# Optimization experiments

Hardware: AMD Instinct MI355X
Metric: run time of the kernel (lower is better)

Reference implementation:

```python
import jax, jax.numpy as jnp
import numpy as np

V, EMB, HID, ENC = 32000, 512, 1024, 1024
B, T, TB = 64, 512, 512
PAD = 0


def setup_inputs() -> dict:
    key = jax.random.key(0)
    kk = jax.random.split(key, 24)
    w = lambda k, s: jax.random.normal(k, s, dtype=jnp.float32) * 0.02
    a = lambda k, s: jax.random.normal(k, s, dtype=jnp.float32)
    emb_table = w(kk[0], (V, EMB)).at[PAD].set(0.0)  # padding_idx row zeroed
    IN = EMB + ENC + HID  # lstm input size
    return {
        "y": jax.random.randint(kk[1], (B,), 0, V),
        "h": a(kk[2], (B, HID)),
        "c": a(kk[3], (B, HID)),
        "enc_out": a(kk[4], (B, T, ENC)),
        "bwd_states": a(kk[5], (B, TB, HID)),
        "src_ids": jax.random.randint(kk[6], (B, T), 0, V),
        "src_mask": jnp.ones((B, T), dtype=jnp.int32),
        "emb_table": emb_table,
        "W_ih": w(kk[7], (4 * HID, IN)),
        "W_hh": w(kk[8], (4 * HID, HID)),
        "b_ih": jnp.zeros((4 * HID,), jnp.float32),
        "b_hh": jnp.zeros((4 * HID,), jnp.float32),
        "Wq_e": w(kk[9], (HID, HID)),
        "Wk_e": w(kk[10], (HID, ENC)),
        "v_e": w(kk[11], (HID,)),
        "Wq_b": w(kk[12], (HID, HID)),
        "Wk_b": w(kk[13], (HID, HID)),
        "v_b": w(kk[14], (HID,)),
        "Wp": w(kk[15], (V, HID)),
        "bp": jnp.zeros((V,), jnp.float32),
        "wc": w(kk[16], (ENC,)),
        "ws": w(kk[17], (HID,)),
        "wy": w(kk[18], (EMB,)),
        "pg_b": jnp.zeros((), jnp.float32),
    }


def _bahdanau(query, keys, Wq, Wk, v, mask=None):
    # query [B,H], keys [B,T,D] -> context [B,D], attn [B,T]
    q = query @ Wq.T                                  # [B,A]
    k = jnp.einsum("btd,ad->bta", keys, Wk)           # [B,T,A]
    e = jnp.einsum("bta,a->bt", jnp.tanh(q[:, None, :] + k), v)
    if mask is not None:
        e = jnp.where(mask == 0, jnp.finfo(e.dtype).min, e)
    attn = jax.nn.softmax(e, axis=-1)
    ctx = jnp.einsum("bt,btd->bd", attn, keys)
    return ctx, attn


def reference(y, h, c, enc_out, bwd_states, src_ids, src_mask, emb_table,
              W_ih, W_hh, b_ih, b_hh, Wq_e, Wk_e, v_e, Wq_b, Wk_b, v_b,
              Wp, bp, wc, ws, wy, pg_b):
    emb = emb_table[y]                                # [B,EMB]
    query = h                                         # state[0].squeeze(0)
    c_enc, attn_enc = _bahdanau(query, enc_out, Wq_e, Wk_e, v_e, src_mask)
    c_bwd, _ = _bahdanau(query, bwd_states, Wq_b, Wk_b, v_b)
    x = jnp.concatenate([emb, c_enc, c_bwd], axis=-1)  # [B,EMB+ENC+HID]
    gates = x @ W_ih.T + h @ W_hh.T + b_ih + b_hh      # [B,4H], torch order i,f,g,o
    i, f, g, o = jnp.split(gates, 4, axis=-1)
    c_new = jax.nn.sigmoid(f) * c + jax.nn.sigmoid(i) * jnp.tanh(g)
    h_new = jax.nn.sigmoid(o) * jnp.tanh(c_new)
    vocab_dist = jax.nn.softmax(h_new @ Wp.T + bp, axis=-1)  # [B,V]
    p_gen = jax.nn.sigmoid(c_enc @ wc + h_new @ ws + emb @ wy + pg_b)[:, None]
    p_vocab = p_gen * vocab_dist
    copy_mask = (src_ids < V).astype(vocab_dist.dtype)
    safe_ids = jnp.minimum(src_ids, V - 1)
    contrib = (1.0 - p_gen) * attn_enc * copy_mask     # [B,T]
    scatter = jax.vmap(lambda idx, val: jnp.zeros((V,), val.dtype).at[idx].add(val))(safe_ids, contrib)
    final_dist = p_vocab + scatter
    return final_dist, h_new, c_new
```

## Files before the change

### kernel.cpp

```cpp
#include <hip/hip_runtime.h>
#include <hip/hip_bf16.h>

#define VSZ   32000
#define EMBD  512
#define HIDD  1024
#define BB    64
#define TSEQ  512
#define G4    4096

typedef short bf16x8 __attribute__((ext_vector_type(8)));
typedef float f32x4  __attribute__((ext_vector_type(4)));

typedef __attribute__((address_space(3))) unsigned       lds_u32_t;
typedef __attribute__((address_space(1))) const unsigned glb_u32_t;
__device__ __forceinline__ void gload16(const void* g, void* l){
  __builtin_amdgcn_global_load_lds((glb_u32_t*)g, (lds_u32_t*)l, 16, 0, 0);
}

__device__ __forceinline__ float sigmoid_f(float x){ return 1.0f/(1.0f+__expf(-x)); }
__device__ __forceinline__ float fast_tanh(float x){
  float e = __expf(2.0f*x);
  return 1.0f - 2.0f*__builtin_amdgcn_rcpf(e + 1.0f);
}
__device__ __forceinline__ short f2bfs(float x){
  unsigned u = __float_as_uint(x);
  unsigned r = (u + 0x7FFFu + ((u>>16)&1u)) >> 16;
  return (short)r;
}
__device__ __forceinline__ float bf2f(short s){
  return __uint_as_float(((unsigned)(unsigned short)s) << 16);
}
__device__ __forceinline__ unsigned cvtpk(float a, float b){
  unsigned r;
  asm("v_cvt_pk_bf16_f32 %0, %1, %2" : "=v"(r) : "v"(a), "v"(b));
  return r;
}
__device__ __forceinline__ bf16x8 cvt8(float4 a, float4 b){
  union { unsigned u[4]; bf16x8 v; } o;
  o.u[0]=cvtpk(a.x,a.y); o.u[1]=cvtpk(a.z,a.w);
  o.u[2]=cvtpk(b.x,b.y); o.u[3]=cvtpk(b.z,b.w);
  return o.v;
}
__device__ __forceinline__ float wave_sum(float x){
  #pragma unroll
  for (int off=32; off>0; off>>=1) x += __shfl_xor(x, off);
  return x;
}
__device__ __forceinline__ float wave_max(float x){
  #pragma unroll
  for (int off=32; off>0; off>>=1) x = fmaxf(x, __shfl_xor(x, off));
  return x;
}

__global__ __launch_bounds__(256) void k_pack(const float* __restrict__ Wk,
                                              short* __restrict__ dst){
  int id = blockIdx.x*256 + threadIdx.x;
  int a = id >> 7, g = id & 127;
  int gs = (g & ~7) | ((g & 7) ^ (a & 7));
  const float* src = Wk + (size_t)a*1024 + gs*8;
  float4 f0 = ((const float4*)src)[0], f1 = ((const float4*)src)[1];
  *(bf16x8*)(dst + (size_t)id*8) = cvt8(f0, f1);
}

__global__ __launch_bounds__(256) void k_cvtkeys(const float* __restrict__ enc,
                                                 const float* __restrict__ bwd,
                                                 short* __restrict__ dst){
  int att = blockIdx.y;
  const float* src0 = att ? bwd : enc;
  int id = blockIdx.x*256 + threadIdx.x;
  int g = id & 127, bt = id >> 7;
  int t = bt & 511;
  int gs = (g & ~7) | ((g & 7) ^ (t & 7));
  const float* sp = src0 + (size_t)bt*1024 + gs*8;
  float4 f0 = ((const float4*)sp)[0], f1 = ((const float4*)sp)[1];
  *(bf16x8*)(dst + (((size_t)att*32768 + bt)*128 + g)*8) = cvt8(f0, f1);
}

__global__ __launch_bounds__(256) void k_prep_h(const float* __restrict__ h,
                                                short* __restrict__ xb){
  int id = blockIdx.x*256 + threadIdx.x;
  int b = id >> 7, d = (id & 127)*8;
  const float4* s = (const float4*)(h + (size_t)b*HIDD + d);
  *(bf16x8*)(xb + (size_t)b*3584 + 2560 + d) = cvt8(s[0], s[1]);
}

__global__ __launch_bounds__(256) void k_prep_x2(const float* __restrict__ tab,
                                                 const int* __restrict__ y,
                                                 const float* __restrict__ ctxe,
                                                 const float* __restrict__ ctxb,
                                                 short* __restrict__ xb){
  int id = blockIdx.x*256 + threadIdx.x;
  if (id >= 64*320) return;
  int b = id / 320, off = (id % 320)*8;
  const float* src;
  if (off < 512)        src = tab  + (size_t)y[b]*EMBD + off;
  else if (off < 1536)  src = ctxe + (size_t)b*HIDD + (off-512);
  else                  src = ctxb + (size_t)b*HIDD + (off-1536);
  float4 f0 = ((const float4*)src)[0], f1 = ((const float4*)src)[1];
  *(bf16x8*)(xb + (size_t)b*3584 + off) = cvt8(f0, f1);
}

__global__ __launch_bounds__(256) void k_mm64(
    const short* __restrict__ A0, int lda0, const float* __restrict__ B0, int ldb0, int K0, float* __restrict__ out0, int ldo0,
    const short* __restrict__ A1, int lda1, const float* __restrict__ B1, int ldb1, int K1, float* __restrict__ out1, int ldo1){
  const short* A; const float* B; float* out; int lda, ldb, K, ldo;
  if (blockIdx.z == 0){ A=A0; B=B0; out=out0; lda=lda0; ldb=ldb0; K=K0; ldo=ldo0; }
  else                { A=A1; B=B1; out=out1; lda=lda1; ldb=ldb1; K=K1; ldo=ldo1; }
  int tid = threadIdx.x, l = tid & 63, w = tid >> 6;
  int l15 = l & 15, l4 = l >> 4;
  int n0 = blockIdx.x*256 + w*64;
  int kper = K / gridDim.y;
  int dbeg = blockIdx.y * kper, dend = dbeg + kper;
  f32x4 acc[4][4];
  #pragma unroll
  for (int i=0;i<4;i++)
    #pragma unroll
    for (int j=0;j<4;j++)
      #pragma unroll
      for (int r=0;r<4;r++) acc[i][j][r]=0.f;
  for (int d0=dbeg; d0<dend; d0+=32){
    bf16x8 af[4];
    #pragma unroll
    for (int ms=0; ms<4; ms++)
      af[ms] = *(const bf16x8*)(A + (size_t)(ms*16 + l15)*lda + d0 + l4*8);
    bf16x8 bfr[4];
    #pragma unroll
    for (int ni=0; ni<4; ni++){
      const float* bp = B + (size_t)(n0 + ni*16 + l15)*ldb + d0 + l4*8;
      float4 f0 = ((const float4*)bp)[0], f1 = ((const float4*)bp)[1];
      bfr[ni] = cvt8(f0, f1);
    }
    #pragma unroll
    for (int ms=0; ms<4; ms++)
      #pragma unroll
      for (int ni=0; ni<4; ni++)
        acc[ms][ni] = __builtin_amdgcn_mfma_f32_16x16x32_bf16(af[ms], bfr[ni], acc[ms][ni], 0,0,0);
  }
  float* op = out + (size_t)blockIdx.y * 64 * ldo;
  #pragma unroll
  for (int ms=0; ms<4; ms++)
    #pragma unroll
    for (int ni=0; ni<4; ni++)
      #pragma unroll
      for (int r=0; r<4; r++){
        int m = ms*16 + l4*4 + r;
        op[(size_t)m*ldo + n0 + ni*16 + l15] = acc[ms][ni][r];
      }
}

__global__ __launch_bounds__(256,3) void k_energy(
    const short* __restrict__ pkeys,
    const short* __restrict__ pke, const short* __restrict__ pkb,
    const float* __restrict__ qpe, const float* __restrict__ qpb,
    const float* __restrict__ ve, const float* __restrict__ vb,
    float* __restrict__ ep_out){
  __shared__ short A_s[128*64];
  __shared__ short B_s[128*64];
  __shared__ float ebuf[2][128];

  int wg = blockIdx.x;
  int xcd = wg & 7, idx = wg >> 3;
  int tglob = xcd*64 + (idx >> 3);
  int A0 = idx & 7;
  int att = tglob >> 8;
  int tt  = tglob & 255;
  int b = tt >> 2, t0 = (tt & 3)*128;

  const short* pk = att ? pkb : pke;
  const float* qp = att ? qpb : qpe;
  const float* v  = att ? vb  : ve;

  int tid = threadIdx.x, l = tid & 63, w = tid >> 6;
  int l15 = l & 15, l4 = l >> 4;
  int wr = w >> 1, wc = w & 1;

  const char* asrc = (const char*)(pkeys + ((size_t)att*32768 + (size_t)b*512)*1024)
                   + (size_t)(t0 + w*32 + (l>>3))*2048 + (l&7)*16;
  const char* bsrc = (const char*)pk + (size_t)(A0*128 + w*32 + (l>>3))*2048 + (l&7)*16;

  f32x4 acc[4][4];
  #pragma unroll
  for (int i=0;i<4;i++)
    #pragma unroll
    for (int j=0;j<4;j++)
      #pragma unroll
      for (int r=0;r<4;r++) acc[i][j][r]=0.f;

  for (int c=0; c<16; ++c){
    if (c) __syncthreads();
    #pragma unroll
    for (int k=0;k<4;k++)
      gload16(asrc + (size_t)c*128 + (size_t)k*16384, (char*)A_s + w*4096 + k*1024);
    #pragma unroll
    for (int k=0;k<4;k++)
      gload16(bsrc + (size_t)c*128 + (size_t)k*16384, (char*)B_s + w*4096 + k*1024);
    __syncthreads();
    #pragma unroll
    for (int ks=0; ks<2; ks++){
      bf16x8 af[4], bf[4];
      #pragma unroll
      for (int ms=0; ms<4; ms++){
        int row = wr*64 + ms*16 + l15;
        af[ms] = *(const bf16x8*)((char*)A_s + row*128 + ((ks*64 + l4*16) ^ ((row&7)<<4)));
      }
      #pragma unroll
      for (int ni=0; ni<4; ni++){
        int row = wc*64 + ni*16 + l15;
        bf[ni] = *(const bf16x8*)((char*)B_s + row*128 + ((ks*64 + l4*16) ^ ((row&7)<<4)));
      }
      #pragma unroll
      for (int ms=0; ms<4; ms++)
        #pragma unroll
        for (int ni=0; ni<4; ni++)
          acc[ms][ni] = __builtin_amdgcn_mfma_f32_16x16x32_bf16(af[ms], bf[ni], acc[ms][ni], 0,0,0);
    }
  }

  float qv[4], vv[4];
  #pragma unroll
  for (int ni=0; ni<4; ni++){
    int a = A0*128 + wc*64 + ni*16 + l15;
    qv[ni] = qp[(size_t)b*HIDD + a] + qp[65536 + (size_t)b*HIDD + a];
    vv[ni] = v[a];
  }
  float es[16];
  #pragma unroll
  for (int ms=0; ms<4; ms++)
    #pragma unroll
    for (int r=0; r<4; r++){
      float s = 0.f;
      #pragma unroll
      for (int ni=0; ni<4; ni++)
        s += vv[ni]*fast_tanh(qv[ni] + acc[ms][ni][r]);
      es[ms*4+r] = s;
    }
  #pragma unroll
  for (int i=0;i<16;i++){
    float x = es[i];
    x += __shfl_xor(x,1); x += __shfl_xor(x,2);
    x += __shfl_xor(x,4); x += __shfl_xor(x,8);
    es[i] = x;
  }
  if (l15 == 0){
    #pragma unroll
    for (int ms=0; ms<4; ms++)
      #pragma unroll
      for (int r=0; r<4; r++)
        ebuf[wc][wr*64 + ms*16 + l4*4 + r] = es[ms*4+r];
  }
  __syncthreads();
  if (tid < 128)
    ep_out[(((size_t)att*8 + A0)*BB + b)*TSEQ + t0 + tid] = ebuf[0][tid] + ebuf[1][tid];
}

__global__ __launch_bounds__(256) void k_softmax_t(const float* __restrict__ ep,
                                                   const int* __restrict__ mask,
                                                   float* __restrict__ att_e,
                                                   float* __restrict__ att_b){
  int b = blockIdx.x, att = blockIdx.y;
  float* e = (att ? att_b : att_e) + (size_t)b*TSEQ;
  __shared__ float red[8];
  int tid = threadIdx.x, lane = tid & 63, w = tid >> 6;
  float v0 = 0.f, v1 = 0.f;
  #pragma unroll
  for (int i=0;i<8;i++){
    const float* p = ep + (((size_t)att*8 + i)*BB + b)*TSEQ;
    v0 += p[tid]; v1 += p[tid+256];
  }
  if (att==0){
    if (mask[(size_t)b*TSEQ + tid]==0)      v0 = -3.4e38f;
    if (mask[(size_t)b*TSEQ + tid+256]==0)  v1 = -3.4e38f;
  }
  float m = wave_max(fmaxf(v0, v1));
  if (lane==0) red[w] = m;
  __syncthreads();
  m = fmaxf(fmaxf(red[0],red[1]), fmaxf(red[2],red[3]));
  float x0 = __expf(v0-m), x1 = __expf(v1-m);
  float s = wave_sum(x0+x1);
  if (lane==0) red[4+w] = s;
  __syncthreads();
  s = red[4]+red[5]+red[6]+red[7];
  float inv = 1.0f/s;
  e[tid] = x0*inv; e[tid+256] = x1*inv;
}

__global__ __launch_bounds__(256) void k_ctx(const short* __restrict__ pkeys,
                                             const float* __restrict__ att_e,
                                             const float* __restrict__ att_b,
                                             float* __restrict__ ctxp){
  int b = blockIdx.x, sel = blockIdx.y, s = blockIdx.z;
  const short* base = pkeys + (((size_t)sel*32768) + (size_t)b*512 + s*64)*1024;
  const float* att  = (sel ? att_b : att_e) + (size_t)b*TSEQ + s*64;
  int g = threadIdx.x & 127, th = threadIdx.x >> 7;
  const short* rp = base + (size_t)th*32*1024;
  float acc[8];
  #pragma unroll
  for (int j=0;j<8;j++) acc[j]=0.f;
  for (int t=0;t<32;t++){
    float a = att[th*32 + t];
    int gg = (g & ~7) | ((g & 7) ^ (t & 7));
    bf16x8 kv = *(const bf16x8*)(rp + (size_t)t*1024 + gg*8);
    #pragma unroll
    for (int j=0;j<8;j++) acc[j] += a*bf2f(kv[j]);
  }
  float* o = ctxp + ((((size_t)sel*BB + b)*16) + s*2 + th)*1024 + g*8;
  float4 o0, o1;
  o0.x=acc[0]; o0.y=acc[1]; o0.z=acc[2]; o0.w=acc[3];
  o1.x=acc[4]; o1.y=acc[5]; o1.z=acc[6]; o1.w=acc[7];
  ((float4*)o)[0] = o0; ((float4*)o)[1] = o1;
}

__global__ __launch_bounds__(256) void k_ctxred(const float* __restrict__ ctxp,
                                                float* __restrict__ ctx_e,
                                                float* __restrict__ ctx_b){
  int id = blockIdx.x*256 + threadIdx.x;
  int sel = id >> 16; int rem = id & 65535; int b = rem >> 10; int d = rem & 1023;
  const float* p = ctxp + (((size_t)sel*BB + b)*16)*1024 + d;
  float s = 0.f;
  #pragma unroll
  for (int i=0;i<16;i++) s += p[i*1024];
  (sel ? ctx_b : ctx_e)[(size_t)b*HIDD + d] = s;
}

__global__ __launch_bounds__(256) void k_lstm(const float* __restrict__ gp,
                                              const float* __restrict__ b_ih,
                                              const float* __restrict__ b_hh,
                                              const float* __restrict__ c_old,
                                              float* __restrict__ out,
                                              short* __restrict__ hb){
  int id = blockIdx.x*256 + threadIdx.x;
  int b = id >> 10, j = id & 1023;
  size_t base = (size_t)b*G4;
  float gs[4];
  #pragma unroll
  for (int g=0; g<4; g++){
    int col = g*1024 + j;
    float s = b_ih[col] + b_hh[col];
    #pragma unroll
    for (int k=0;k<8;k++) s += gp[(size_t)k*(64*G4) + base + col];
    gs[g] = s;
  }
  float ig = sigmoid_f(gs[0]);
  float fg = sigmoid_f(gs[1]);
  float gg = tanhf(gs[2]);
  float og = sigmoid_f(gs[3]);
  float cn = fg*c_old[id] + ig*gg;
  float hn = og*tanhf(cn);
  out[(size_t)BB*VSZ + id] = hn;
  out[(size_t)BB*VSZ + (size_t)BB*HIDD + id] = cn;
  hb[id] = f2bfs(hn);
}

__global__ __launch_bounds__(256) void k_vocab2(const short* __restrict__ hb,
                                                const float* __restrict__ Wp,
                                                const float* __restrict__ bp,
                                                float* __restrict__ out){
  int tid = threadIdx.x, l = tid & 63, w = tid >> 6;
  int l15 = l & 15, l4 = l >> 4;
  int mh = w >> 1;
  int n0 = blockIdx.x*128 + (w&1)*64;
  f32x4 acc[2][4];
  #pragma unroll
  for (int i=0;i<2;i++)
    #pragma unroll
    for (int j=0;j<4;j++)
      #pragma unroll
      for (int r=0;r<4;r++) acc[i][j][r]=0.f;
  for (int d0=0; d0<1024; d0+=32){
    bf16x8 af[2];
    #pragma unroll
    for (int ms=0; ms<2; ms++)
      af[ms] = *(const bf16x8*)(hb + (size_t)(mh*32 + ms*16 + l15)*1024 + d0 + l4*8);
    bf16x8 bfr[4];
    #pragma unroll
    for (int ni=0; ni<4; ni++){
      const float* bpp = Wp + (size_t)(n0 + ni*16 + l15)*1024 + d0 + l4*8;
      float4 f0 = ((const float4*)bpp)[0], f1 = ((const float4*)bpp)[1];
      bfr[ni] = cvt8(f0, f1);
    }
    #pragma unroll
    for (int ms=0; ms<2; ms++)
      #pragma unroll
      for (int ni=0; ni<4; ni++)
        acc[ms][ni] = __builtin_amdgcn_mfma_f32_16x16x32_bf16(af[ms], bfr[ni], acc[ms][ni], 0,0,0);
  }
  #pragma unroll
  for (int ms=0; ms<2; ms++)
    #pragma unroll
    for (int ni=0; ni<4; ni++)
      #pragma unroll
      for (int r=0; r<4; r++){
        int m = mh*32 + ms*16 + l4*4 + r;
        int n = n0 + ni*16 + l15;
        out[(size_t)m*VSZ + n] = acc[ms][ni][r] + bp[n];
      }
}

__global__ __launch_bounds__(1024) void k_final(const float* __restrict__ ctxe,
                                                const float* __restrict__ tab,
                                                const int* __restrict__ y,
                                                const float* __restrict__ wc,
                                                const float* __restrict__ wsv,
                                                const float* __restrict__ wy,
                                                const float* __restrict__ pgb,
                                                float* __restrict__ out,
                                                float* __restrict__ pgen_ws){
  __shared__ float red[32];
  int b = blockIdx.x, tid = threadIdx.x, lane = tid & 63, w = tid >> 6;
  const float* hn = out + (size_t)BB*VSZ + (size_t)b*HIDD;
  float acc = ctxe[(size_t)b*HIDD + tid]*wc[tid] + hn[tid]*wsv[tid];
  if (tid < 512) acc += tab[(size_t)y[b]*EMBD + tid]*wy[tid];
  acc = wave_sum(acc);
  if (lane==0) red[w] = acc;
  __syncthreads();
  float s0 = pgb[0];
  #pragma unroll
  for (int i=0;i<16;i++) s0 += red[i];
  float pg = sigmoid_f(s0);
  if (tid==0) pgen_ws[b] = pg;
  __syncthreads();

  float* row = out + (size_t)b*VSZ;
  float m = -3.4e38f;
  for (int i=tid;i<VSZ;i+=1024) m = fmaxf(m, row[i]);
  m = wave_max(m);
  if (lane==0) red[w] = m;
  __syncthreads();
  #pragma unroll
  for (int i=0;i<16;i++) m = fmaxf(m, red[i]);
  float s = 0.f;
  for (int i=tid;i<VSZ;i+=1024) s += __expf(row[i]-m);
  s = wave_sum(s);
  if (lane==0) red[16+w] = s;
  __syncthreads();
  float tot = 0.f;
  #pragma unroll
  for (int i=0;i<16;i++) tot += red[16+i];
  float scale = pg / tot;
  for (int i=tid;i<VSZ;i+=1024) row[i] = __expf(row[i]-m)*scale;
}

__global__ __launch_bounds__(256) void k_scatter(const int* __restrict__ src_ids,
                                                 const float* __restrict__ att_e,
                                                 const float* __restrict__ pgen_ws,
                                                 float* __restrict__ out){
  int id = blockIdx.x*256 + threadIdx.x;
  int b = id >> 9;
  float pg = pgen_ws[b];
  int sid = src_ids[id];
  float contrib = (1.0f - pg) * att_e[id] * (sid < VSZ ? 1.0f : 0.0f);
  int safe = sid < VSZ-1 ? sid : VSZ-1;
  atomicAdd(&out[(size_t)b*VSZ + safe], contrib);
}

extern "C" void kernel_launch(void* const* d_in, const int* in_sizes, int n_in,
                              void* d_out, int out_size, void* d_ws, size_t ws_size,
                              hipStream_t stream){
  const int*   y     = (const int*)d_in[0];
  const float* h     = (const float*)d_in[1];
  const float* c     = (const float*)d_in[2];
  const float* enc   = (const float*)d_in[3];
  const float* bwd   = (const float*)d_in[4];
  const int*   sids  = (const int*)d_in[5];
  const int*   smask = (const int*)d_in[6];
  const float* tab   = (const float*)d_in[7];
  const float* W_ih  = (const float*)d_in[8];
  const float* W_hh  = (const float*)d_in[9];
  const float* b_ih  = (const float*)d_in[10];
  const float* b_hh  = (const float*)d_in[11];
  const float* Wq_e  = (const float*)d_in[12];
  const float* Wk_e  = (const float*)d_in[13];
  const float* v_e   = (const float*)d_in[14];
  const float* Wq_b  = (const float*)d_in[15];
  const float* Wk_b  = (const float*)d_in[16];
  const float* v_b   = (const float*)d_in[17];
  const float* Wp    = (const float*)d_in[18];
  const float* bp    = (const float*)d_in[19];
  const float* wc    = (const float*)d_in[20];
  const float* wsv   = (const float*)d_in[21];
  const float* wy    = (const float*)d_in[22];
  const float* pgb   = (const float*)d_in[23];
  float* out = (float*)d_out;

  float* W = (float*)d_ws;
  float* ws_qpe  = W; W += 2*BB*HIDD;
  float* ws_qpb  = W; W += 2*BB*HIDD;
  float* ws_ep   = W; W += 2*8*BB*TSEQ;
  float* ws_atte = W; W += BB*TSEQ;
  float* ws_attb = W; W += BB*TSEQ;
  float* ws_ctxe = W; W += BB*HIDD;
  float* ws_ctxb = W; W += BB*HIDD;
  float* ws_ctxp = W; W += 2*BB*16*1024;
  float* ws_pgen = W; W += 64;
  float* ws_gp   = W; W += 8*BB*G4;
  short* xb      = (short*)W; W += (BB*3584)/2;
  short* hb      = (short*)W; W += (BB*HIDD)/2;
  short* pk_e    = (short*)W; W += (HIDD*HIDD)/2;
  short* pk_b    = (short*)W; W += (HIDD*HIDD)/2;
  short* pkeys   = (short*)W; W += (2*BB*TSEQ*HIDD)/2;

  k_pack<<<512, 256, 0, stream>>>(Wk_e, pk_e);
  k_pack<<<512, 256, 0, stream>>>(Wk_b, pk_b);
  k_cvtkeys<<<dim3(16384,2), 256, 0, stream>>>(enc, bwd, pkeys);
  k_prep_h<<<32, 256, 0, stream>>>(h, xb);
  k_mm64<<<dim3(4,2,2), 256, 0, stream>>>(
      xb+2560, 3584, Wq_e, 1024, 1024, ws_qpe, 1024,
      xb+2560, 3584, Wq_b, 1024, 1024, ws_qpb, 1024);
  k_energy<<<4096, 256, 0, stream>>>(pkeys, pk_e, pk_b,
      ws_qpe, ws_qpb, v_e, v_b, ws_ep);
  k_softmax_t<<<dim3(BB,2), 256, 0, stream>>>(ws_ep, smask, ws_atte, ws_attb);
  k_ctx<<<dim3(BB,2,8), 256, 0, stream>>>(pkeys, ws_atte, ws_attb, ws_ctxp);
  k_ctxred<<<512, 256, 0, stream>>>(ws_ctxp, ws_ctxe, ws_ctxb);
  k_prep_x2<<<80, 256, 0, stream>>>(tab, y, ws_ctxe, ws_ctxb, xb);
  k_mm64<<<dim3(16,4,2), 256, 0, stream>>>(
      xb,      3584, W_ih, 2560, 2560, ws_gp,             G4,
      xb+2560, 3584, W_hh, 1024, 1024, ws_gp + 4*BB*G4,   G4);
  k_lstm<<<256, 256, 0, stream>>>(ws_gp, b_ih, b_hh, c, out, hb);
  k_vocab2<<<250, 256, 0, stream>>>(hb, Wp, bp, out);
  k_final<<<BB, 1024, 0, stream>>>(ws_ctxe, tab, y, wc, wsv, wy, pgb, out, ws_pgen);
  k_scatter<<<128, 256, 0, stream>>>(sids, ws_atte, ws_pgen, out);
}
```

Baseline: 391.6 us.

## Merge prep kernels and split vocab softmax into segmented reduce and scale

```diff
diff --git a/kernel.cpp b/kernel.cpp
--- a/kernel.cpp
+++ b/kernel.cpp
@@ -52,36 +52,39 @@
   return x;
 }
 
-__global__ __launch_bounds__(256) void k_pack(const float* __restrict__ Wk,
-                                              short* __restrict__ dst){
-  int id = blockIdx.x*256 + threadIdx.x;
-  int a = id >> 7, g = id & 127;
-  int gs = (g & ~7) | ((g & 7) ^ (a & 7));
-  const float* src = Wk + (size_t)a*1024 + gs*8;
-  float4 f0 = ((const float4*)src)[0], f1 = ((const float4*)src)[1];
-  *(bf16x8*)(dst + (size_t)id*8) = cvt8(f0, f1);
-}
-
-__global__ __launch_bounds__(256) void k_cvtkeys(const float* __restrict__ enc,
-                                                 const float* __restrict__ bwd,
-                                                 short* __restrict__ dst){
-  int att = blockIdx.y;
-  const float* src0 = att ? bwd : enc;
-  int id = blockIdx.x*256 + threadIdx.x;
-  int g = id & 127, bt = id >> 7;
-  int t = bt & 511;
-  int gs = (g & ~7) | ((g & 7) ^ (t & 7));
-  const float* sp = src0 + (size_t)bt*1024 + gs*8;
-  float4 f0 = ((const float4*)sp)[0], f1 = ((const float4*)sp)[1];
-  *(bf16x8*)(dst + (((size_t)att*32768 + bt)*128 + g)*8) = cvt8(f0, f1);
-}
-
-__global__ __launch_bounds__(256) void k_prep_h(const float* __restrict__ h,
-                                                short* __restrict__ xb){
-  int id = blockIdx.x*256 + threadIdx.x;
-  int b = id >> 7, d = (id & 127)*8;
-  const float4* s = (const float4*)(h + (size_t)b*HIDD + d);
-  *(bf16x8*)(xb + (size_t)b*3584 + 2560 + d) = cvt8(s[0], s[1]);
+__global__ __launch_bounds__(256) void k_prep_all(
+    const float* __restrict__ Wk_e, const float* __restrict__ Wk_b,
+    const float* __restrict__ enc,  const float* __restrict__ bwd,
+    const float* __restrict__ h,
+    short* __restrict__ pk_e, short* __restrict__ pk_b,
+    short* __restrict__ pkeys, short* __restrict__ xb){
+  int bid = blockIdx.x;
+  if (bid < 1024){
+    const float* Wk = (bid < 512) ? Wk_e : Wk_b;
+    short* dst      = (bid < 512) ? pk_e : pk_b;
+    int id = (bid & 511)*256 + threadIdx.x;
+    int a = id >> 7, g = id & 127;
+    int gs = (g & ~7) | ((g & 7) ^ (a & 7));
+    const float* src = Wk + (size_t)a*1024 + gs*8;
+    float4 f0 = ((const float4*)src)[0], f1 = ((const float4*)src)[1];
+    *(bf16x8*)(dst + (size_t)id*8) = cvt8(f0, f1);
+  } else if (bid < 33792){
+    int r = bid - 1024;
+    int att = r >> 14;
+    const float* src0 = att ? bwd : enc;
+    int id = (r & 16383)*256 + threadIdx.x;
+    int g = id & 127, bt = id >> 7;
+    int t = bt & 511;
+    int gs = (g & ~7) | ((g & 7) ^ (t & 7));
+    const float* sp = src0 + (size_t)bt*1024 + gs*8;
+    float4 f0 = ((const float4*)sp)[0], f1 = ((const float4*)sp)[1];
+    *(bf16x8*)(pkeys + (((size_t)att*32768 + bt)*128 + g)*8) = cvt8(f0, f1);
+  } else {
+    int id = (bid - 33792)*256 + threadIdx.x;
+    int b = id >> 7, d = (id & 127)*8;
+    const float4* s = (const float4*)(h + (size_t)b*HIDD + d);
+    *(bf16x8*)(xb + (size_t)b*3584 + 2560 + d) = cvt8(s[0], s[1]);
+  }
 }
 
 __global__ __launch_bounds__(256) void k_prep_x2(const float* __restrict__ tab,
@@ -396,48 +399,76 @@
       }
 }
 
-__global__ __launch_bounds__(1024) void k_final(const float* __restrict__ ctxe,
-                                                const float* __restrict__ tab,
-                                                const int* __restrict__ y,
-                                                const float* __restrict__ wc,
-                                                const float* __restrict__ wsv,
-                                                const float* __restrict__ wy,
-                                                const float* __restrict__ pgb,
-                                                float* __restrict__ out,
-                                                float* __restrict__ pgen_ws){
-  __shared__ float red[32];
+__global__ __launch_bounds__(256) void k_pgen(const float* __restrict__ ctxe,
+                                              const float* __restrict__ tab,
+                                              const int* __restrict__ y,
+                                              const float* __restrict__ wc,
+                                              const float* __restrict__ wsv,
+                                              const float* __restrict__ wy,
+                                              const float* __restrict__ pgb,
+                                              const float* __restrict__ out,
+                                              float* __restrict__ pgen_ws){
+  __shared__ float red[4];
   int b = blockIdx.x, tid = threadIdx.x, lane = tid & 63, w = tid >> 6;
   const float* hn = out + (size_t)BB*VSZ + (size_t)b*HIDD;
-  float acc = ctxe[(size_t)b*HIDD + tid]*wc[tid] + hn[tid]*wsv[tid];
-  if (tid < 512) acc += tab[(size_t)y[b]*EMBD + tid]*wy[tid];
+  const float* emb = tab + (size_t)y[b]*EMBD;
+  float acc = 0.f;
+  #pragma unroll
+  for (int i=0;i<4;i++){
+    int d = i*256 + tid;
+    acc += ctxe[(size_t)b*HIDD + d]*wc[d] + hn[d]*wsv[d];
+  }
+  #pragma unroll
+  for (int i=0;i<2;i++){
+    int d = i*256 + tid;
+    acc += emb[d]*wy[d];
+  }
   acc = wave_sum(acc);
   if (lane==0) red[w] = acc;
   __syncthreads();
-  float s0 = pgb[0];
-  #pragma unroll
-  for (int i=0;i<16;i++) s0 += red[i];
-  float pg = sigmoid_f(s0);
-  if (tid==0) pgen_ws[b] = pg;
-  __syncthreads();
-
-  float* row = out + (size_t)b*VSZ;
+  if (tid==0)
+    pgen_ws[b] = sigmoid_f(red[0]+red[1]+red[2]+red[3] + pgb[0]);
+}
+
+__global__ __launch_bounds__(256) void k_vred(const float* __restrict__ out,
+                                              float* __restrict__ vm,
+                                              float* __restrict__ vs){
+  __shared__ float red[8];
+  int b = blockIdx.x, seg = blockIdx.y;
+  int tid = threadIdx.x, lane = tid & 63, w = tid >> 6;
+  const float* row = out + (size_t)b*VSZ;
+  int lo = seg*8000, hi = lo + 8000;
   float m = -3.4e38f;
-  for (int i=tid;i<VSZ;i+=1024) m = fmaxf(m, row[i]);
+  for (int i=lo+tid; i<hi; i+=256) m = fmaxf(m, row[i]);
   m = wave_max(m);
   if (lane==0) red[w] = m;
   __syncthreads();
-  #pragma unroll
-  for (int i=0;i<16;i++) m = fmaxf(m, red[i]);
+  m = fmaxf(fmaxf(red[0],red[1]), fmaxf(red[2],red[3]));
   float s = 0.f;
-  for (int i=tid;i<VSZ;i+=1024) s += __expf(row[i]-m);
+  for (int i=lo+tid; i<hi; i+=256) s += __expf(row[i]-m);
   s = wave_sum(s);
-  if (lane==0) red[16+w] = s;
+  if (lane==0) red[4+w] = s;
   __syncthreads();
-  float tot = 0.f;
-  #pragma unroll
-  for (int i=0;i<16;i++) tot += red[16+i];
-  float scale = pg / tot;
-  for (int i=tid;i<VSZ;i+=1024) row[i] = __expf(row[i]-m)*scale;
+  if (tid==0){
+    vm[b*4+seg] = m;
+    vs[b*4+seg] = red[4]+red[5]+red[6]+red[7];
+  }
+}
+
+__global__ __launch_bounds__(256) void k_vscale(float* __restrict__ out,
+                                                const float* __restrict__ vm,
+                                                const float* __restrict__ vs,
+                                                const float* __restrict__ pgen_ws){
+  int b = blockIdx.x, seg = blockIdx.y;
+  int tid = threadIdx.x;
+  float m0=vm[b*4+0], m1=vm[b*4+1], m2=vm[b*4+2], m3=vm[b*4+3];
+  float M = fmaxf(fmaxf(m0,m1), fmaxf(m2,m3));
+  float S = vs[b*4+0]*__expf(m0-M) + vs[b*4+1]*__expf(m1-M)
+          + vs[b*4+2]*__expf(m2-M) + vs[b*4+3]*__expf(m3-M);
+  float scale = pgen_ws[b] / S;
+  float* row = out + (size_t)b*VSZ;
+  int lo = seg*8000, hi = lo + 8000;
+  for (int i=lo+tid; i<hi; i+=256) row[i] = __expf(row[i]-M)*scale;
 }
 
 __global__ __launch_bounds__(256) void k_scatter(const int* __restrict__ src_ids,
@@ -492,6 +523,8 @@
   float* ws_ctxb = W; W += BB*HIDD;
   float* ws_ctxp = W; W += 2*BB*16*1024;
   float* ws_pgen = W; W += 64;
+  float* ws_vm   = W; W += 256;
+  float* ws_vs   = W; W += 256;
   float* ws_gp   = W; W += 8*BB*G4;
   short* xb      = (short*)W; W += (BB*3584)/2;
   short* hb      = (short*)W; W += (BB*HIDD)/2;
@@ -499,10 +532,8 @@
   short* pk_b    = (short*)W; W += (HIDD*HIDD)/2;
   short* pkeys   = (short*)W; W += (2*BB*TSEQ*HIDD)/2;
 
-  k_pack<<<512, 256, 0, stream>>>(Wk_e, pk_e);
-  k_pack<<<512, 256, 0, stream>>>(Wk_b, pk_b);
-  k_cvtkeys<<<dim3(16384,2), 256, 0, stream>>>(enc, bwd, pkeys);
-  k_prep_h<<<32, 256, 0, stream>>>(h, xb);
+  k_prep_all<<<33824, 256, 0, stream>>>(Wk_e, Wk_b, enc, bwd, h,
+      pk_e, pk_b, pkeys, xb);
   k_mm64<<<dim3(4,2,2), 256, 0, stream>>>(
       xb+2560, 3584, Wq_e, 1024, 1024, ws_qpe, 1024,
       xb+2560, 3584, Wq_b, 1024, 1024, ws_qpb, 1024);
@@ -517,6 +548,8 @@
       xb+2560, 3584, W_hh, 1024, 1024, ws_gp + 4*BB*G4,   G4);
   k_lstm<<<256, 256, 0, stream>>>(ws_gp, b_ih, b_hh, c, out, hb);
   k_vocab2<<<250, 256, 0, stream>>>(hb, Wp, bp, out);
-  k_final<<<BB, 1024, 0, stream>>>(ws_ctxe, tab, y, wc, wsv, wy, pgb, out, ws_pgen);
+  k_pgen<<<BB, 256, 0, stream>>>(ws_ctxe, tab, y, wc, wsv, wy, pgb, out, ws_pgen);
+  k_vred<<<dim3(BB,4), 256, 0, stream>>>(out, ws_vm, ws_vs);
+  k_vscale<<<dim3(BB,4), 256, 0, stream>>>(out, ws_vm, ws_vs, ws_pgen);
   k_scatter<<<128, 256, 0, stream>>>(sids, ws_atte, ws_pgen, out);
 }
```

New measurement: 387.4 us. About the same (-1.1%).
